# Kernel tuning notes

Measured on AMD Instinct MI355X. Metric: run time of the kernel, lower is better.

The kernel has to match this reference:

```python
import jax, jax.numpy as jnp
import numpy as np

NEG_BIG = -9e15
ALPHA = 0.2  # leaky relu slope


def setup_inputs() -> dict:
    key = jax.random.key(0)
    k_h, k_adj, k_W, k_a = jax.random.split(key, 4)
    N, F_in, F_out = 8192, 512, 64
    h = jax.random.normal(k_h, (N, F_in), dtype=jnp.float32)
    adj = jax.random.randint(k_adj, (N, N), 0, 2, dtype=jnp.int32)
    adj = adj.at[jnp.arange(N), jnp.arange(N)].set(1)  # self-loops (add_self_loops)
    # xavier_uniform with gain=1.414
    limW = 1.414 * np.sqrt(6.0 / (F_in + F_out))
    W = jax.random.uniform(k_W, (F_in, F_out), jnp.float32, -limW, limW)
    lima = 1.414 * np.sqrt(6.0 / (2 * F_out + 1))
    a = jax.random.uniform(k_a, (2 * F_out, 1), jnp.float32, -lima, lima)
    return {"h": h, "adj": adj, "W": W, "a": a}


def reference(h, adj, W, a):
    F_out = W.shape[1]
    Wh = h @ W                                  # [N, F_out]
    # a_input[i,j] = concat(Wh[i], Wh[j]); a_input @ a == Wh@a1 + (Wh@a2)^T
    a1, a2 = a[:F_out, 0], a[F_out:, 0]
    src = Wh @ a1                               # [N]
    dst = Wh @ a2                               # [N]
    e = jax.nn.leaky_relu(src[:, None] + dst[None, :], ALPHA)  # [N, N]
    att = jnp.where(adj > 0, e, NEG_BIG)
    att = jax.nn.softmax(att, axis=1)
    # dropout is identity in eval mode (training=False)
    return att @ Wh                             # [N, F_out]
```

## Files before the change

### kernel.cpp

```cpp
#include <hip/hip_runtime.h>
#include <hip/hip_bf16.h>

#define N 8192
#define FIN 512
#define FOUT 64
#define L2E 1.44269504089f

typedef __attribute__((address_space(1))) const void* gas_cptr;
typedef __attribute__((address_space(3))) void* las_ptr;
typedef float f32x4 __attribute__((ext_vector_type(4)));
typedef short bf16x8 __attribute__((ext_vector_type(8)));

#if __has_builtin(__builtin_amdgcn_exp2f)
#define EXP2(x) __builtin_amdgcn_exp2f(x)
#else
#define EXP2(x) exp2f(x)
#endif

static __device__ __forceinline__ unsigned short f2bf_rne(float f) {
  unsigned u = __float_as_uint(f);
  u += 0x7FFFu + ((u >> 16) & 1u);
  return (unsigned short)(u >> 16);
}
static __device__ __forceinline__ unsigned fkey(float f) {
  unsigned u = __float_as_uint(f);
  return (u & 0x80000000u) ? ~u : (u | 0x80000000u);
}

__global__ __launch_bounds__(256) void k_wh(
    const float* __restrict__ h, const float* __restrict__ W,
    const float* __restrict__ a, unsigned short* __restrict__ WhT,
    float* __restrict__ src2, float* __restrict__ dst2,
    unsigned* __restrict__ dmaxk) {
  __shared__ float hs[32][68];
  __shared__ float wsh[64][68];
  const int t = threadIdx.x;
  const int row0 = blockIdx.x * 32;
  const int rg = t >> 4;
  const int cg = t & 15;
  float acc[2][4];
#pragma unroll
  for (int i = 0; i < 2; ++i)
#pragma unroll
    for (int q = 0; q < 4; ++q) acc[i][q] = 0.f;

  for (int kc = 0; kc < FIN; kc += 64) {
#pragma unroll
    for (int i = 0; i < 2; ++i) {
      int idx = t + i * 256;
      int r = idx >> 4, c4 = idx & 15;
      *reinterpret_cast<float4*>(&hs[r][c4 * 4]) =
          *reinterpret_cast<const float4*>(&h[(size_t)(row0 + r) * FIN + kc + c4 * 4]);
    }
#pragma unroll
    for (int i = 0; i < 4; ++i) {
      int idx = t + i * 256;
      int r = idx >> 4, c4 = idx & 15;
      *reinterpret_cast<float4*>(&wsh[r][c4 * 4]) =
          *reinterpret_cast<const float4*>(&W[(size_t)(kc + r) * FOUT + c4 * 4]);
    }
    __syncthreads();
#pragma unroll 8
    for (int k = 0; k < 64; ++k) {
      float4 b = *reinterpret_cast<const float4*>(&wsh[k][cg * 4]);
      float a0 = hs[rg * 2 + 0][k];
      float a1 = hs[rg * 2 + 1][k];
      acc[0][0] += a0 * b.x; acc[0][1] += a0 * b.y; acc[0][2] += a0 * b.z; acc[0][3] += a0 * b.w;
      acc[1][0] += a1 * b.x; acc[1][1] += a1 * b.y; acc[1][2] += a1 * b.z; acc[1][3] += a1 * b.w;
    }
    __syncthreads();
  }

  float s2l[2];
#pragma unroll
  for (int i = 0; i < 2; ++i) {
    int row = row0 + rg * 2 + i;
    float s1 = acc[i][0] * a[cg * 4 + 0] + acc[i][1] * a[cg * 4 + 1] +
               acc[i][2] * a[cg * 4 + 2] + acc[i][3] * a[cg * 4 + 3];
    float s2 = acc[i][0] * a[FOUT + cg * 4 + 0] + acc[i][1] * a[FOUT + cg * 4 + 1] +
               acc[i][2] * a[FOUT + cg * 4 + 2] + acc[i][3] * a[FOUT + cg * 4 + 3];
#pragma unroll
    for (int msk = 8; msk >= 1; msk >>= 1) {
      s1 += __shfl_xor(s1, msk);
      s2 += __shfl_xor(s2, msk);
    }
    s1 *= L2E; s2 *= L2E;
    if (cg == 0) { src2[row] = s1; dst2[row] = s2; }
    s2l[i] = s2;
  }
#pragma unroll
  for (int q = 0; q < 4; ++q) {
    ushort2 pr = make_ushort2(f2bf_rne(acc[0][q]), f2bf_rne(acc[1][q]));
    *reinterpret_cast<ushort2*>(&WhT[(size_t)(cg * 4 + q) * N + row0 + rg * 2]) = pr;
  }
  float wmax = fmaxf(s2l[0], s2l[1]);
#pragma unroll
  for (int msk = 1; msk <= 32; msk <<= 1) wmax = fmaxf(wmax, __shfl_xor(wmax, msk));
  if ((t & 63) == 0) atomicMax(dmaxk, fkey(wmax));
}

__global__ __launch_bounds__(256) void k_attn(
    const int* __restrict__ adj, const unsigned short* __restrict__ WhT,
    const float* __restrict__ src2, const float* __restrict__ dst2,
    const unsigned* __restrict__ dmaxk, float* __restrict__ out,
    float* __restrict__ Opart, float* __restrict__ lpart, const int split) {
  __shared__ __attribute__((aligned(16))) unsigned short whs[64 * 64];
  __shared__ __attribute__((aligned(16))) unsigned short pbs[64 * 64];

  const int t = threadIdx.x;
  const int w = t >> 6;
  const int ll = t & 63;
  const int rg = t >> 4;
  const int cg = t & 15;
  const int i0 = rg * 4;
  const int row0 = blockIdx.x * 64;
  const int jlen = N / split;
  const int jbase = blockIdx.y * jlen;
  const int ntiles = jlen / 64;

  unsigned kk = dmaxk[0];
  float dmax2 = (kk & 0x80000000u) ? __uint_as_float(kk & 0x7FFFFFFFu)
                                   : __uint_as_float(~kk);

  float s2v[4], m2[4], l[4];
#pragma unroll
  for (int r = 0; r < 4; ++r) {
    s2v[r] = src2[row0 + i0 + r];
    float x = s2v[r] + dmax2;
    m2[r] = fmaxf(x, 0.2f * x);
    l[r] = 0.f;
  }

  f32x4 acc[4];
#pragma unroll
  for (int c = 0; c < 4; ++c) acc[c] = (f32x4){0.f, 0.f, 0.f, 0.f};

  int av[4][4];
  float dv[4];
  {
    const int j0 = jbase;
#pragma unroll
    for (int r = 0; r < 4; ++r) {
      int4 x = *reinterpret_cast<const int4*>(&adj[(size_t)(row0 + i0 + r) * N + j0 + cg * 4]);
      av[r][0] = x.x; av[r][1] = x.y; av[r][2] = x.z; av[r][3] = x.w;
    }
    float4 d4 = *reinterpret_cast<const float4*>(&dst2[j0 + cg * 4]);
    dv[0] = d4.x; dv[1] = d4.y; dv[2] = d4.z; dv[3] = d4.w;
  }

  for (int jt = 0; jt < ntiles; ++jt) {
    const int j0 = jbase + jt * 64;

#pragma unroll
    for (int i = 0; i < 2; ++i) {
      int slot = t + i * 256;
      int b = slot * 16;
      int u = b ^ (((b >> 7) & 7) << 4);
      int f = u >> 7;
      int jl = (u & 127) >> 1;
      const unsigned short* gsrc = &WhT[(size_t)f * N + j0 + jl];
      __builtin_amdgcn_global_load_lds((gas_cptr)gsrc,
                                       (las_ptr)((char*)whs + b), 16, 0, 0);
    }

    float p[4][4];
#pragma unroll
    for (int r = 0; r < 4; ++r) {
#pragma unroll
      for (int jj = 0; jj < 4; ++jj) {
        float x = s2v[r] + dv[jj];
        float e2 = fmaxf(x, 0.2f * x);
        float pe = EXP2(e2 - m2[r]);
        pe = av[r][jj] > 0 ? pe : 0.f;
        p[r][jj] = pe;
        l[r] += pe;
      }
    }
#pragma unroll
    for (int r = 0; r < 4; ++r) {
      unsigned u0 = __float_as_uint(p[r][0]);
      unsigned u1 = __float_as_uint(p[r][1]);
      unsigned u2 = __float_as_uint(p[r][2]);
      unsigned u3 = __float_as_uint(p[r][3]);
      uint2 pk = make_uint2((u0 >> 16) | (u1 & 0xFFFF0000u),
                            (u2 >> 16) | (u3 & 0xFFFF0000u));
      int row = i0 + r;
      int ba = (row << 7) + (cg << 3);
      ba ^= (row & 7) << 4;
      *reinterpret_cast<uint2*>((char*)pbs + ba) = pk;
    }
    __syncthreads();

    {
      const int jn = (jt + 1 < ntiles) ? (j0 + 64) : j0;
#pragma unroll
      for (int r = 0; r < 4; ++r) {
        int4 x = *reinterpret_cast<const int4*>(&adj[(size_t)(row0 + i0 + r) * N + jn + cg * 4]);
        av[r][0] = x.x; av[r][1] = x.y; av[r][2] = x.z; av[r][3] = x.w;
      }
      float4 d4 = *reinterpret_cast<const float4*>(&dst2[jn + cg * 4]);
      dv[0] = d4.x; dv[1] = d4.y; dv[2] = d4.z; dv[3] = d4.w;
    }

    {
      const int lc = ll & 15;
      const int g16 = (ll >> 4) << 4;
#pragma unroll
      for (int k0 = 0; k0 < 2; ++k0) {
        int arow = 16 * w + lc;
        int ab = (arow << 7) + k0 * 64 + g16;
        ab ^= (arow & 7) << 4;
        bf16x8 afrag = *reinterpret_cast<const bf16x8*>((const char*)pbs + ab);
#pragma unroll
        for (int c = 0; c < 4; ++c) {
          int brow = c * 16 + lc;
          int bb = (brow << 7) + k0 * 64 + g16;
          bb ^= (brow & 7) << 4;
          bf16x8 bfrag = *reinterpret_cast<const bf16x8*>((const char*)whs + bb);
          acc[c] = __builtin_amdgcn_mfma_f32_16x16x32_bf16(afrag, bfrag, acc[c], 0, 0, 0);
        }
      }
    }
    __syncthreads();
  }

#pragma unroll
  for (int msk = 8; msk >= 1; msk >>= 1)
#pragma unroll
    for (int r = 0; r < 4; ++r) l[r] += __shfl_xor(l[r], msk);

  const int orow = row0 + 16 * w + ((ll >> 4) << 2);
  const int ocol = ll & 15;
  if (split == 1) {
#pragma unroll
    for (int c = 0; c < 4; ++c)
#pragma unroll
      for (int q = 0; q < 4; ++q)
        out[(size_t)(orow + q) * FOUT + c * 16 + ocol] = acc[c][q] / l[q];
  } else {
    const int pb = blockIdx.y;
#pragma unroll
    for (int c = 0; c < 4; ++c)
#pragma unroll
      for (int q = 0; q < 4; ++q)
        Opart[((size_t)pb * N + orow + q) * FOUT + c * 16 + ocol] = acc[c][q];
    if (cg == 0) {
#pragma unroll
      for (int r = 0; r < 4; ++r)
        lpart[(size_t)pb * N + row0 + i0 + r] = l[r];
    }
  }
}

__global__ __launch_bounds__(256) void k_combine(
    const float* __restrict__ Opart, const float* __restrict__ lpart,
    float* __restrict__ out, const int split) {
  int idx = blockIdx.x * 256 + threadIdx.x;
  int row = idx >> 6;
  float num = 0.f, den = 0.f;
  for (int k = 0; k < split; ++k) {
    num += Opart[(size_t)k * N * FOUT + idx];
    den += lpart[(size_t)k * N + row];
  }
  out[idx] = num / den;
}

extern "C" void kernel_launch(void* const* d_in, const int* in_sizes, int n_in,
                              void* d_out, int out_size, void* d_ws, size_t ws_size,
                              hipStream_t stream) {
  const float* h = (const float*)d_in[0];
  const int* adj = (const int*)d_in[1];
  const float* W = (const float*)d_in[2];
  const float* a = (const float*)d_in[3];
  float* out = (float*)d_out;

  unsigned short* WhT = (unsigned short*)d_ws;
  float* src2 = (float*)(WhT + (size_t)FOUT * N);
  float* dst2 = src2 + N;
  unsigned* dmaxk = (unsigned*)(dst2 + N);
  float* Opart = (float*)(dmaxk + 64);

  const size_t base_bytes = (size_t)FOUT * N * 2 + 2 * N * 4 + 256;
  int split = 8;
  while (split > 1 &&
         base_bytes + (size_t)split * ((size_t)N * FOUT + N) * 4 > ws_size)
    split >>= 1;
  float* lpart = Opart + (size_t)split * N * FOUT;

  hipMemsetAsync(dmaxk, 0, 4, stream);
  k_wh<<<dim3(N / 32), 256, 0, stream>>>(h, W, a, WhT, src2, dst2, dmaxk);
  k_attn<<<dim3(N / 64, split), 256, 0, stream>>>(adj, WhT, src2, dst2, dmaxk,
                                                  out, Opart, lpart, split);
  if (split > 1)
    k_combine<<<dim3((N * FOUT) / 256), 256, 0, stream>>>(Opart, lpart, out, split);
}
```

Before: 110.6 us.

## Use bf16 MFMA for h@W projection and double-buffer attention tiles

```diff
diff --git a/kernel.cpp b/kernel.cpp
--- a/kernel.cpp
+++ b/kernel.cpp
@@ -5,6 +5,7 @@
 #define FIN 512
 #define FOUT 64
 #define L2E 1.44269504089f
+#define SPLIT 8
 
 typedef __attribute__((address_space(1))) const void* gas_cptr;
 typedef __attribute__((address_space(3))) void* las_ptr;
@@ -32,71 +33,130 @@
     const float* __restrict__ a, unsigned short* __restrict__ WhT,
     float* __restrict__ src2, float* __restrict__ dst2,
     unsigned* __restrict__ dmaxk) {
-  __shared__ float hs[32][68];
-  __shared__ float wsh[64][68];
+  __shared__ __attribute__((aligned(16))) char wts[64 * 512 * 2];
+  __shared__ __attribute__((aligned(16))) char hsb[2][64 * 64 * 2];
+
   const int t = threadIdx.x;
-  const int row0 = blockIdx.x * 32;
-  const int rg = t >> 4;
-  const int cg = t & 15;
-  float acc[2][4];
-#pragma unroll
-  for (int i = 0; i < 2; ++i)
-#pragma unroll
-    for (int q = 0; q < 4; ++q) acc[i][q] = 0.f;
-
-  for (int kc = 0; kc < FIN; kc += 64) {
-#pragma unroll
-    for (int i = 0; i < 2; ++i) {
-      int idx = t + i * 256;
-      int r = idx >> 4, c4 = idx & 15;
-      *reinterpret_cast<float4*>(&hs[r][c4 * 4]) =
-          *reinterpret_cast<const float4*>(&h[(size_t)(row0 + r) * FIN + kc + c4 * 4]);
-    }
-#pragma unroll
-    for (int i = 0; i < 4; ++i) {
-      int idx = t + i * 256;
-      int r = idx >> 4, c4 = idx & 15;
-      *reinterpret_cast<float4*>(&wsh[r][c4 * 4]) =
-          *reinterpret_cast<const float4*>(&W[(size_t)(kc + r) * FOUT + c4 * 4]);
-    }
-    __syncthreads();
-#pragma unroll 8
-    for (int k = 0; k < 64; ++k) {
-      float4 b = *reinterpret_cast<const float4*>(&wsh[k][cg * 4]);
-      float a0 = hs[rg * 2 + 0][k];
-      float a1 = hs[rg * 2 + 1][k];
-      acc[0][0] += a0 * b.x; acc[0][1] += a0 * b.y; acc[0][2] += a0 * b.z; acc[0][3] += a0 * b.w;
-      acc[1][0] += a1 * b.x; acc[1][1] += a1 * b.y; acc[1][2] += a1 * b.z; acc[1][3] += a1 * b.w;
-    }
-    __syncthreads();
-  }
-
-  float s2l[2];
-#pragma unroll
-  for (int i = 0; i < 2; ++i) {
-    int row = row0 + rg * 2 + i;
-    float s1 = acc[i][0] * a[cg * 4 + 0] + acc[i][1] * a[cg * 4 + 1] +
-               acc[i][2] * a[cg * 4 + 2] + acc[i][3] * a[cg * 4 + 3];
-    float s2 = acc[i][0] * a[FOUT + cg * 4 + 0] + acc[i][1] * a[FOUT + cg * 4 + 1] +
-               acc[i][2] * a[FOUT + cg * 4 + 2] + acc[i][3] * a[FOUT + cg * 4 + 3];
-#pragma unroll
-    for (int msk = 8; msk >= 1; msk >>= 1) {
-      s1 += __shfl_xor(s1, msk);
-      s2 += __shfl_xor(s2, msk);
-    }
-    s1 *= L2E; s2 *= L2E;
-    if (cg == 0) { src2[row] = s1; dst2[row] = s2; }
-    s2l[i] = s2;
-  }
+  const int w = t >> 6;
+  const int ll = t & 63;
+  const int lc = ll & 15;
+  const int row0 = blockIdx.x * 64;
+
+  {
+    const int k0 = t * 2;
+#pragma unroll
+    for (int f4 = 0; f4 < 16; ++f4) {
+      float4 x0 = *reinterpret_cast<const float4*>(&W[(size_t)k0 * FOUT + f4 * 4]);
+      float4 x1 = *reinterpret_cast<const float4*>(&W[(size_t)(k0 + 1) * FOUT + f4 * 4]);
+      const float e0[4] = {x0.x, x0.y, x0.z, x0.w};
+      const float e1[4] = {x1.x, x1.y, x1.z, x1.w};
+#pragma unroll
+      for (int e = 0; e < 4; ++e) {
+        int f = f4 * 4 + e;
+        int bb = f * 1024 + k0 * 2;
+        bb ^= (f & 7) << 4;
+        *reinterpret_cast<ushort2*>(wts + bb) =
+            make_ushort2(f2bf_rne(e0[e]), f2bf_rne(e1[e]));
+      }
+    }
+  }
+  __syncthreads();
+
+  f32x4 acc[4];
+#pragma unroll
+  for (int c = 0; c < 4; ++c) acc[c] = (f32x4){0.f, 0.f, 0.f, 0.f};
+
+  const int hrow = 16 * w + (ll >> 2);
+  const float* hbase = &h[(size_t)(row0 + hrow) * FIN + (ll & 3) * 16];
+
+#define LOADH(dst, kc)                                                        \
+  do {                                                                        \
+    dst[0] = *reinterpret_cast<const float4*>(hbase + (kc));                  \
+    dst[1] = *reinterpret_cast<const float4*>(hbase + (kc) + 4);              \
+    dst[2] = *reinterpret_cast<const float4*>(hbase + (kc) + 8);              \
+    dst[3] = *reinterpret_cast<const float4*>(hbase + (kc) + 12);             \
+  } while (0)
+
+#define WRITEH(buf, src)                                                      \
+  do {                                                                        \
+    int bb0 = hrow * 128 + (ll & 3) * 32;                                     \
+    bb0 ^= (hrow & 7) << 4;                                                   \
+    _Pragma("unroll") for (int q = 0; q < 4; ++q) {                           \
+      ushort4 u = make_ushort4(f2bf_rne(src[q].x), f2bf_rne(src[q].y),        \
+                               f2bf_rne(src[q].z), f2bf_rne(src[q].w));       \
+      *reinterpret_cast<ushort4*>(hsb[buf] + (bb0 ^ (q * 8))) = u;            \
+    }                                                                         \
+  } while (0)
+
+#define MFMA_CHUNK(buf, kcb)                                                  \
+  do {                                                                        \
+    _Pragma("unroll") for (int k0 = 0; k0 < 2; ++k0) {                        \
+      int arow = 16 * w + lc;                                                 \
+      int ab = arow * 128 + k0 * 64 + ((ll >> 4) << 4);                       \
+      ab ^= (arow & 7) << 4;                                                  \
+      bf16x8 af = *reinterpret_cast<const bf16x8*>(hsb[buf] + ab);            \
+      _Pragma("unroll") for (int c = 0; c < 4; ++c) {                         \
+        int f = c * 16 + lc;                                                  \
+        int bb = f * 1024 + (kcb) + k0 * 64 + ((ll >> 4) << 4);               \
+        bb ^= (f & 7) << 4;                                                   \
+        bf16x8 bfr = *reinterpret_cast<const bf16x8*>(wts + bb);              \
+        acc[c] = __builtin_amdgcn_mfma_f32_16x16x32_bf16(af, bfr, acc[c], 0, 0, 0); \
+      }                                                                       \
+    }                                                                         \
+  } while (0)
+
+  float4 ha[4], hb[4];
+  LOADH(ha, 0);
+#pragma unroll
+  for (int c2 = 0; c2 < 4; ++c2) {
+    WRITEH(0, ha);
+    LOADH(hb, (2 * c2 + 1) * 64);
+    MFMA_CHUNK(0, (2 * c2) * 128);
+    WRITEH(1, hb);
+    if (c2 < 3) LOADH(ha, (2 * c2 + 2) * 64);
+    MFMA_CHUNK(1, (2 * c2 + 1) * 128);
+  }
+
+  float a1v[4], a2v[4];
+#pragma unroll
+  for (int c = 0; c < 4; ++c) {
+    a1v[c] = a[c * 16 + lc];
+    a2v[c] = a[FOUT + c * 16 + lc];
+  }
+  float p1[4], p2[4];
 #pragma unroll
   for (int q = 0; q < 4; ++q) {
-    ushort2 pr = make_ushort2(f2bf_rne(acc[0][q]), f2bf_rne(acc[1][q]));
-    *reinterpret_cast<ushort2*>(&WhT[(size_t)(cg * 4 + q) * N + row0 + rg * 2]) = pr;
-  }
-  float wmax = fmaxf(s2l[0], s2l[1]);
-#pragma unroll
-  for (int msk = 1; msk <= 32; msk <<= 1) wmax = fmaxf(wmax, __shfl_xor(wmax, msk));
-  if ((t & 63) == 0) atomicMax(dmaxk, fkey(wmax));
+    p1[q] = acc[0][q] * a1v[0] + acc[1][q] * a1v[1] + acc[2][q] * a1v[2] + acc[3][q] * a1v[3];
+    p2[q] = acc[0][q] * a2v[0] + acc[1][q] * a2v[1] + acc[2][q] * a2v[2] + acc[3][q] * a2v[3];
+  }
+#pragma unroll
+  for (int msk = 8; msk >= 1; msk >>= 1)
+#pragma unroll
+    for (int q = 0; q < 4; ++q) {
+      p1[q] += __shfl_xor(p1[q], msk);
+      p2[q] += __shfl_xor(p2[q], msk);
+    }
+#pragma unroll
+  for (int q = 0; q < 4; ++q) { p1[q] *= L2E; p2[q] *= L2E; }
+
+  const int r0 = row0 + 16 * w + ((ll >> 4) << 2);
+  if (lc == 0) {
+#pragma unroll
+    for (int q = 0; q < 4; ++q) { src2[r0 + q] = p1[q]; dst2[r0 + q] = p2[q]; }
+  }
+#pragma unroll
+  for (int c = 0; c < 4; ++c) {
+    ushort4 u = make_ushort4(f2bf_rne(acc[c][0]), f2bf_rne(acc[c][1]),
+                             f2bf_rne(acc[c][2]), f2bf_rne(acc[c][3]));
+    *reinterpret_cast<ushort4*>(&WhT[(size_t)(c * 16 + lc) * N + r0]) = u;
+  }
+  float wm = fmaxf(fmaxf(p2[0], p2[1]), fmaxf(p2[2], p2[3]));
+  wm = fmaxf(wm, __shfl_xor(wm, 16));
+  wm = fmaxf(wm, __shfl_xor(wm, 32));
+  if (ll == 0) atomicMax(dmaxk, fkey(wm));
+#undef LOADH
+#undef WRITEH
+#undef MFMA_CHUNK
 }
 
 __global__ __launch_bounds__(256) void k_attn(
@@ -104,8 +164,8 @@
     const float* __restrict__ src2, const float* __restrict__ dst2,
     const unsigned* __restrict__ dmaxk, float* __restrict__ out,
     float* __restrict__ Opart, float* __restrict__ lpart, const int split) {
-  __shared__ __attribute__((aligned(16))) unsigned short whs[64 * 64];
-  __shared__ __attribute__((aligned(16))) unsigned short pbs[64 * 64];
+  __shared__ __attribute__((aligned(16))) char whs[2 * 8192];
+  __shared__ __attribute__((aligned(16))) char pbs[8192];
 
   const int t = threadIdx.x;
   const int w = t >> 6;
@@ -119,8 +179,8 @@
   const int ntiles = jlen / 64;
 
   unsigned kk = dmaxk[0];
-  float dmax2 = (kk & 0x80000000u) ? __uint_as_float(kk & 0x7FFFFFFFu)
-                                   : __uint_as_float(~kk);
+  const float dmax2 = (kk & 0x80000000u) ? __uint_as_float(kk & 0x7FFFFFFFu)
+                                         : __uint_as_float(~kk);
 
   float s2v[4], m2[4], l[4];
 #pragma unroll
@@ -135,32 +195,43 @@
 #pragma unroll
   for (int c = 0; c < 4; ++c) acc[c] = (f32x4){0.f, 0.f, 0.f, 0.f};
 
-  int av[4][4];
-  float dv[4];
-  {
-    const int j0 = jbase;
-#pragma unroll
-    for (int r = 0; r < 4; ++r) {
-      int4 x = *reinterpret_cast<const int4*>(&adj[(size_t)(row0 + i0 + r) * N + j0 + cg * 4]);
-      av[r][0] = x.x; av[r][1] = x.y; av[r][2] = x.z; av[r][3] = x.w;
-    }
-    float4 d4 = *reinterpret_cast<const float4*>(&dst2[j0 + cg * 4]);
-    dv[0] = d4.x; dv[1] = d4.y; dv[2] = d4.z; dv[3] = d4.w;
-  }
+#define STAGE_WHS(buf, j0)                                                    \
+  do {                                                                        \
+    _Pragma("unroll") for (int i_ = 0; i_ < 2; ++i_) {                        \
+      int slot = t + i_ * 256;                                                \
+      int b = slot * 16;                                                      \
+      int u = b ^ (((b >> 7) & 7) << 4);                                      \
+      int f_ = u >> 7;                                                        \
+      int jl = (u & 127) >> 1;                                                \
+      __builtin_amdgcn_global_load_lds(                                       \
+          (gas_cptr)(WhT + (size_t)f_ * N + (j0) + jl),                       \
+          (las_ptr)(whs + (buf)*8192 + b), 16, 0, 0);                         \
+    }                                                                         \
+  } while (0)
+
+#define LOAD_ADJ(AV, DV, j0)                                                  \
+  do {                                                                        \
+    _Pragma("unroll") for (int r_ = 0; r_ < 4; ++r_) {                        \
+      int4 x_ = *reinterpret_cast<const int4*>(                               \
+          &adj[(size_t)(row0 + i0 + r_) * N + (j0) + cg * 4]);                \
+      AV[r_][0] = x_.x; AV[r_][1] = x_.y; AV[r_][2] = x_.z; AV[r_][3] = x_.w; \
+    }                                                                         \
+    float4 d_ = *reinterpret_cast<const float4*>(&dst2[(j0) + cg * 4]);       \
+    DV[0] = d_.x; DV[1] = d_.y; DV[2] = d_.z; DV[3] = d_.w;                   \
+  } while (0)
+
+  int av[4][4], nav[4][4];
+  float dv[4], ndv[4];
+  STAGE_WHS(0, jbase);
+  LOAD_ADJ(av, dv, jbase);
 
   for (int jt = 0; jt < ntiles; ++jt) {
-    const int j0 = jbase + jt * 64;
-
-#pragma unroll
-    for (int i = 0; i < 2; ++i) {
-      int slot = t + i * 256;
-      int b = slot * 16;
-      int u = b ^ (((b >> 7) & 7) << 4);
-      int f = u >> 7;
-      int jl = (u & 127) >> 1;
-      const unsigned short* gsrc = &WhT[(size_t)f * N + j0 + jl];
-      __builtin_amdgcn_global_load_lds((gas_cptr)gsrc,
-                                       (las_ptr)((char*)whs + b), 16, 0, 0);
+    const int cur = jt & 1;
+    __syncthreads();
+
+    if (jt + 1 < ntiles) {
+      STAGE_WHS(cur ^ 1, jbase + (jt + 1) * 64);
+      LOAD_ADJ(nav, ndv, jbase + (jt + 1) * 64);
     }
 
     float p[4][4];
@@ -187,19 +258,7 @@
       int row = i0 + r;
       int ba = (row << 7) + (cg << 3);
       ba ^= (row & 7) << 4;
-      *reinterpret_cast<uint2*>((char*)pbs + ba) = pk;
-    }
-    __syncthreads();
-
-    {
-      const int jn = (jt + 1 < ntiles) ? (j0 + 64) : j0;
-#pragma unroll
-      for (int r = 0; r < 4; ++r) {
-        int4 x = *reinterpret_cast<const int4*>(&adj[(size_t)(row0 + i0 + r) * N + jn + cg * 4]);
-        av[r][0] = x.x; av[r][1] = x.y; av[r][2] = x.z; av[r][3] = x.w;
-      }
-      float4 d4 = *reinterpret_cast<const float4*>(&dst2[jn + cg * 4]);
-      dv[0] = d4.x; dv[1] = d4.y; dv[2] = d4.z; dv[3] = d4.w;
+      *reinterpret_cast<uint2*>(pbs + ba) = pk;
     }
 
     {
@@ -210,18 +269,26 @@
         int arow = 16 * w + lc;
         int ab = (arow << 7) + k0 * 64 + g16;
         ab ^= (arow & 7) << 4;
-        bf16x8 afrag = *reinterpret_cast<const bf16x8*>((const char*)pbs + ab);
+        bf16x8 af = *reinterpret_cast<const bf16x8*>(pbs + ab);
 #pragma unroll
         for (int c = 0; c < 4; ++c) {
           int brow = c * 16 + lc;
           int bb = (brow << 7) + k0 * 64 + g16;
           bb ^= (brow & 7) << 4;
-          bf16x8 bfrag = *reinterpret_cast<const bf16x8*>((const char*)whs + bb);
-          acc[c] = __builtin_amdgcn_mfma_f32_16x16x32_bf16(afrag, bfrag, acc[c], 0, 0, 0);
+          bf16x8 bfr = *reinterpret_cast<const bf16x8*>(whs + cur * 8192 + bb);
+          acc[c] = __builtin_amdgcn_mfma_f32_16x16x32_bf16(af, bfr, acc[c], 0, 0, 0);
         }
       }
     }
-    __syncthreads();
+
+    if (jt + 1 < ntiles) {
+#pragma unroll
+      for (int r = 0; r < 4; ++r) {
+#pragma unroll
+        for (int jj = 0; jj < 4; ++jj) av[r][jj] = nav[r][jj];
+        dv[r] = ndv[r];
+      }
+    }
   }
 
 #pragma unroll
@@ -250,6 +317,8 @@
         lpart[(size_t)pb * N + row0 + i0 + r] = l[r];
     }
   }
+#undef STAGE_WHS
+#undef LOAD_ADJ
 }
 
 __global__ __launch_bounds__(256) void k_combine(
@@ -281,14 +350,14 @@
   float* Opart = (float*)(dmaxk + 64);
 
   const size_t base_bytes = (size_t)FOUT * N * 2 + 2 * N * 4 + 256;
-  int split = 8;
+  int split = SPLIT;
   while (split > 1 &&
          base_bytes + (size_t)split * ((size_t)N * FOUT + N) * 4 > ws_size)
     split >>= 1;
   float* lpart = Opart + (size_t)split * N * FOUT;
 
   hipMemsetAsync(dmaxk, 0, 4, stream);
-  k_wh<<<dim3(N / 32), 256, 0, stream>>>(h, W, a, WhT, src2, dst2, dmaxk);
+  k_wh<<<dim3(N / 64), 256, 0, stream>>>(h, W, a, WhT, src2, dst2, dmaxk);
   k_attn<<<dim3(N / 64, split), 256, 0, stream>>>(adj, WhT, src2, dst2, dmaxk,
                                                   out, Opart, lpart, split);
   if (split > 1)
```

Measured after the change: 107.1 us. 1.03x faster.
